# Performance work log

Hardware: AMD Instinct MI355X
Metric: run time of the kernel (lower is better)

## Reference

```python
import jax, jax.numpy as jnp
import numpy as np

N = 200000          # number of nodes (objects)
H = 64              # hidden_size
ARITIES = [1, 2, 3] # arity per relation
NTUP = [250000, 250000, 250000]  # ground atoms per relation


def setup_inputs() -> dict:
    key = jax.random.key(0)
    ks = jax.random.split(key, 32)
    inp = {"node_states": jax.random.normal(ks[0], (N, H), jnp.float32)}
    i = 1
    for r, (a, t) in enumerate(zip(ARITIES, NTUP)):
        inp[f"rel{r}_idx"] = jax.random.randint(ks[i], (t * a,), 0, N, dtype=jnp.int32).astype(jnp.int64); i += 1
        d = a * H
        s = (2.0 / d) ** 0.5
        inp[f"w1_r{r}"] = jax.random.normal(ks[i], (d, d), jnp.float32) * s; i += 1
        inp[f"b1_r{r}"] = jnp.zeros((d,), jnp.float32)
        inp[f"w2_r{r}"] = jax.random.normal(ks[i], (d, d), jnp.float32) * s; i += 1
        inp[f"b2_r{r}"] = jnp.zeros((d,), jnp.float32)
    su = (1.0 / (2 * H)) ** 0.5
    inp["wu1"] = jax.random.normal(ks[i], (2 * H, 2 * H), jnp.float32) * su; i += 1
    inp["bu1"] = jnp.zeros((2 * H,), jnp.float32)
    inp["wu2"] = jax.random.normal(ks[i], (2 * H, H), jnp.float32) * su
    inp["bu2"] = jnp.zeros((H,), jnp.float32)
    return inp


def reference(node_states, rel0_idx, rel1_idx, rel2_idx,
              w1_r0, b1_r0, w2_r0, b2_r0,
              w1_r1, b1_r1, w2_r1, b2_r1,
              w1_r2, b1_r2, w2_r2, b2_r2,
              wu1, bu1, wu2, bu2):
    sum_msg = jnp.zeros_like(node_states)
    rels = [(ARITIES[0], rel0_idx, w1_r0, b1_r0, w2_r0, b2_r0),
            (ARITIES[1], rel1_idx, w1_r1, b1_r1, w2_r1, b2_r1),
            (ARITIES[2], rel2_idx, w1_r2, b1_r2, w2_r2, b2_r2)]
    for a, idx, w1, b1, w2, b2 in rels:
        # gather node states for each ground atom: [T, a*H]
        x = node_states[idx].reshape(-1, a * H)
        h = jax.nn.relu(x @ w1 + b1)
        msg = (h @ w2 + b2).reshape(-1, H)  # [T*a, H]
        # scatter-add messages back to their nodes
        sum_msg = sum_msg.at[idx].add(msg)
    z = jnp.concatenate([sum_msg, node_states], axis=1)  # [N, 2H]
    return jax.nn.relu(z @ wu1 + bu1) @ wu2 + bu2
```

## Files before the change

kernel.cpp:

```cpp
#include <hip/hip_runtime.h>

#define H 64

typedef __attribute__((ext_vector_type(8))) __bf16 bf16x8;
typedef __attribute__((ext_vector_type(4))) float f32x4;
typedef unsigned short u16;
typedef unsigned int u32;

union F8 { bf16x8 b; u16 u[8]; uint4 q; };

__device__ __forceinline__ u16 f2bf(float f) {
    union { __bf16 h; u16 u; } v; v.h = (__bf16)f; return v.u;
}
__device__ __forceinline__ float bf2f(u16 x) {
    return __uint_as_float((u32)x << 16);
}
__device__ __forceinline__ unsigned swz(int col, int k, int K) {
    return ((unsigned)(col * K + k) * 2u) ^ (((unsigned)col & 7u) << 4);
}

struct Seg { const float* src; unsigned dstBytes; int K; int N; };
struct Segs { Seg s[8]; };

__global__ __launch_bounds__(256) void conv_weights(Segs segs, char* out) {
    Seg sg = segs.s[blockIdx.y];
    int total = sg.K * sg.N;
    char* dst = out + sg.dstBytes;
    for (int e = blockIdx.x * 256 + threadIdx.x; e < total; e += gridDim.x * 256) {
        int k = e / sg.N, n = e % sg.N;
        *(u16*)(dst + swz(n, k, sg.K)) = f2bf(sg.src[e]);
    }
}

__global__ __launch_bounds__(512) void scan_blocks(u32* __restrict__ data,
                                                   u32* __restrict__ sums, int n) {
    __shared__ u32 s[512];
    int tid = threadIdx.x, i = blockIdx.x * 512 + tid;
    u32 v = (i < n) ? data[i] : 0u;
    s[tid] = v; __syncthreads();
    for (int d = 1; d < 512; d <<= 1) {
        u32 t = (tid >= d) ? s[tid - d] : 0u; __syncthreads();
        s[tid] += t; __syncthreads();
    }
    if (i < n) data[i] = s[tid] - v;
    if (tid == 511) sums[blockIdx.x] = s[511];
}

__global__ __launch_bounds__(512) void scan_sums(u32* __restrict__ sums, int nb) {
    __shared__ u32 s[512];
    int tid = threadIdx.x;
    u32 v = (tid < nb) ? sums[tid] : 0u;
    s[tid] = v; __syncthreads();
    for (int d = 1; d < 512; d <<= 1) {
        u32 t = (tid >= d) ? s[tid - d] : 0u; __syncthreads();
        s[tid] += t; __syncthreads();
    }
    if (tid < nb) sums[tid] = s[tid] - v;
}

__global__ __launch_bounds__(512) void scan_add(u32* __restrict__ data,
                                                const u32* __restrict__ sums, int n) {
    int i = blockIdx.x * 512 + threadIdx.x;
    if (i < n) data[i] += sums[blockIdx.x];
}

struct OFix {
    const int* idx0; const int* idx1; const int* idx2;
    int m0, m1, m2;
    const u32* base; const u32* pre; u32* ord;
};

__global__ __launch_bounds__(256) void ord_fix(OFix a) {
    const int Mtot = a.m0 + a.m1 + a.m2;
    for (int e = blockIdx.x * 256 + threadIdx.x; e < Mtot; e += gridDim.x * 256) {
        int lm = e, node;
        if (lm < a.m0) node = a.idx0[lm];
        else { lm -= a.m0; if (lm < a.m1) node = a.idx1[lm]; else node = a.idx2[lm - a.m1]; }
        a.ord[a.base[node] + a.pre[e]] = (u32)e;
    }
}

template<int A>
__device__ __forceinline__ void msg_body(
    const float* __restrict__ ns, const int* __restrict__ idx,
    const u16* __restrict__ w1T, const float* __restrict__ b1,
    const u16* __restrict__ w2T, const float* __restrict__ b2,
    u16* __restrict__ msgR, int T, int bid, u16* Wl, u16* h1)
{
    constexpr int D   = A * 64;
    constexpr int KS  = D / 32;
    constexpr int NT  = D / 16;
    constexpr bool DUAL = (A == 1);
    constexpr int WH  = (A == 3) ? 3 : 1;
    constexpr int NTH = NT / WH;
    constexpr int COLH = D / WH;
    constexpr int NPF = (DUAL ? 2 * D * D : COLH * D) / 8 / 512;

    const int tid  = threadIdx.x;
    const int lane = tid & 63;
    const int w    = tid >> 6;
    const int g    = lane >> 4;
    const int lr   = lane & 15;

    const int tile = bid * 128;
    const int trow = tile + w * 16 + lr;
    const int tl   = trow < T ? trow : T - 1;

    auto stage = [&](const u16* gsrc) {
#pragma unroll
        for (int i = 0; i < NPF; ++i) {
            const u16* gp = gsrc + ((i * 512 + tid) << 3);
            u16* lp = Wl + ((i * 512 + (w << 6)) << 3);
            __builtin_amdgcn_global_load_lds(
                (const __attribute__((address_space(1))) void*)gp,
                (__attribute__((address_space(3))) void*)lp, 16, 0, 0);
        }
    };

    int nodes[A];
#pragma unroll
    for (int s = 0; s < A; ++s) nodes[s] = idx[(long)tl * A + s];

    bf16x8 a1[KS];
#pragma unroll
    for (int kk = 0; kk < KS; ++kk) {
        const float* p = ns + (long)nodes[kk >> 1] * H + ((kk & 1) * 32 + g * 8);
        float4 f0 = *(const float4*)p;
        float4 f1 = *(const float4*)(p + 4);
        F8 t;
        t.u[0] = f2bf(f0.x); t.u[1] = f2bf(f0.y); t.u[2] = f2bf(f0.z); t.u[3] = f2bf(f0.w);
        t.u[4] = f2bf(f1.x); t.u[5] = f2bf(f1.y); t.u[6] = f2bf(f1.z); t.u[7] = f2bf(f1.w);
        a1[kk] = t.b;
    }

    float bias1[NT], bias2[NT];
#pragma unroll
    for (int j = 0; j < NT; ++j) bias1[j] = b1[j * 16 + lr];
#pragma unroll
    for (int j = 0; j < NT; ++j) bias2[j] = b2[j * 16 + lr];

#pragma unroll
    for (int hh = 0; hh < WH; ++hh) {
        stage(DUAL ? w1T : (w1T + (size_t)hh * COLH * D));
        asm volatile("s_waitcnt vmcnt(0)" ::: "memory");
        __syncthreads();

#pragma unroll
        for (int j = 0; j < NTH; ++j) {
            const int jg = hh * NTH + j;
            f32x4 acc = {0.f, 0.f, 0.f, 0.f};
#pragma unroll
            for (int kk = 0; kk < KS; ++kk) {
                F8 bf; bf.q = *(const uint4*)((const char*)Wl + swz(j * 16 + lr, kk * 32 + g * 8, D));
                acc = __builtin_amdgcn_mfma_f32_16x16x32_bf16(a1[kk], bf.b, acc, 0, 0, 0);
            }
#pragma unroll
            for (int r = 0; r < 4; ++r) {
                float vv = acc[r] + bias1[jg];
                vv = vv > 0.f ? vv : 0.f;
                int row = w * 16 + g * 4 + r;
                *(u16*)((char*)h1 + swz(row, jg * 16 + lr, D)) = f2bf(vv);
            }
        }
        if constexpr (!DUAL) __syncthreads();
    }

    bf16x8 a2[KS];
#pragma unroll
    for (int kk = 0; kk < KS; ++kk) {
        int row = w * 16 + lr;
        F8 t; t.q = *(const uint4*)((const char*)h1 + swz(row, kk * 32 + g * 8, D));
        a2[kk] = t.b;
    }

#pragma unroll
    for (int hh = 0; hh < WH; ++hh) {
        if constexpr (!DUAL) {
            stage(w2T + (size_t)hh * COLH * D);
            asm volatile("s_waitcnt vmcnt(0)" ::: "memory");
            __syncthreads();
        }
        const char* W2base = DUAL ? (const char*)(Wl + D * D) : (const char*)Wl;

#pragma unroll
        for (int j = 0; j < NTH; ++j) {
            const int jg = hh * NTH + j;
            f32x4 acc = {0.f, 0.f, 0.f, 0.f};
#pragma unroll
            for (int kk = 0; kk < KS; ++kk) {
                F8 bf; bf.q = *(const uint4*)(W2base + swz(j * 16 + lr, kk * 32 + g * 8, D));
                acc = __builtin_amdgcn_mfma_f32_16x16x32_bf16(a2[kk], bf.b, acc, 0, 0, 0);
            }
            const int gc   = jg * 16 + lr;
            const int slot = gc >> 6;
            const int cs   = gc & 63;
#pragma unroll
            for (int r = 0; r < 4; ++r) {
                int la   = w * 16 + g * 4 + r;
                int mrow = la * A + slot;
                unsigned byte = (((unsigned)(mrow * 64 + cs)) * 2u) ^ (((unsigned)mrow & 7u) << 4);
                *(u16*)((char*)h1 + byte) = f2bf(acc[r] + bias2[jg]);
            }
        }
        if constexpr (!DUAL) { if (hh + 1 < WH) __syncthreads(); }
    }

    const int  mbase = (tile + w * 16) * A;
    const bool full  = (tile + 128 <= T);
#pragma unroll
    for (int i = 0; i < 16 * A; i += 4) {
        int ml   = i + (lane >> 4);
        int mrow = w * 16 * A + ml;
        bool ok  = full || ((tile + w * 16 + ml / A) < T);
        if (ok) {
            unsigned byte = (((unsigned)(mrow * 64 + (lane & 15) * 4)) * 2u) ^ (((unsigned)mrow & 7u) << 4);
            uint2 v = *(const uint2*)((const char*)h1 + byte);
            *(uint2*)(msgR + (size_t)(mbase + ml) * 64 + (lane & 15) * 4) = v;
        }
    }
}

struct MegaA {
    const float* ns;
    const int* idx0; const int* idx1; const int* idx2;
    int m0, m1, m2, t0, t1, t2;
    u32* cnt; u32* pre;
    const u16 *w10, *w20, *w11, *w21, *w12, *w22;
    const float *b10, *b20, *b11, *b21, *b12, *b22;
    u16* msgu;
    int nrank, nb2, nb1, nb0, striped;
};

__global__ __launch_bounds__(512, 4) void mega_kernel(MegaA a) {
    __shared__ __align__(16) u16 sm[36864];
    const int bx = blockIdx.x;
    int kind, id;
    if (a.striped) {
        const int strip = 4 * a.nrank;
        if (bx < strip) {
            if ((bx & 3) == 3) { kind = 1; id = bx >> 2; }
            else               { kind = 0; id = bx - (bx >> 2); }
        } else { kind = 0; id = bx - a.nrank; }
    } else {
        if (bx < a.nrank) { kind = 1; id = bx; }
        else              { kind = 0; id = bx - a.nrank; }
    }

    if (kind == 1) {
        const int Mtot = a.m0 + a.m1 + a.m2;
        for (int e = id * 512 + (int)threadIdx.x; e < Mtot; e += a.nrank * 512) {
            int lm = e, node;
            if (lm < a.m0) node = a.idx0[lm];
            else { lm -= a.m0; if (lm < a.m1) node = a.idx1[lm]; else node = a.idx2[lm - a.m1]; }
            a.pre[e] = atomicAdd(a.cnt + node, 1u);
        }
        return;
    }

    const int nmsg = a.nb2 + a.nb1 + a.nb0;
    if (id >= nmsg) return;
    if (id < a.nb2)
        msg_body<3>(a.ns, a.idx2, a.w12, a.b12, a.w22, a.b22,
                    a.msgu + (size_t)(a.m0 + a.m1) * 64, a.t2, id, sm, sm + 12288);
    else if (id < a.nb2 + a.nb1)
        msg_body<2>(a.ns, a.idx1, a.w11, a.b11, a.w21, a.b21,
                    a.msgu + (size_t)a.m0 * 64, a.t1, id - a.nb2, sm, sm + 16384);
    else
        msg_body<1>(a.ns, a.idx0, a.w10, a.b10, a.w20, a.b20,
                    a.msgu, a.t0, id - a.nb2 - a.nb1, sm, sm + 8192);
}

template<int A>
__global__ __launch_bounds__(512) void rel_kernel(
    const float* __restrict__ ns, const int* __restrict__ idx,
    const u16* __restrict__ w1T, const float* __restrict__ b1,
    const u16* __restrict__ w2T, const float* __restrict__ b2,
    float* __restrict__ dout, int T)
{
    constexpr int D  = A * 64;
    constexpr int KS = D / 32;
    constexpr int NT = D / 16;
    constexpr bool DUAL = (A == 1);
    __shared__ __align__(16) u16 Wl[(DUAL ? 2 : 1) * D * D];
    __shared__ __align__(16) u16 h1[128 * D];

    const int tid  = threadIdx.x;
    const int lane = tid & 63;
    const int w    = tid >> 6;
    const int g    = lane >> 4;
    const int lr   = lane & 15;

    const int tile = blockIdx.x * 128;
    const int trow = tile + w * 16 + lr;
    const int tl   = trow < T ? trow : T - 1;

    {
        constexpr int NV = (DUAL ? 2 : 1) * D * D / 8;
        const uint4* s4 = (const uint4*)w1T;
        uint4* d4 = (uint4*)Wl;
#pragma unroll
        for (int i = 0; i < NV / 512; ++i) d4[i * 512 + tid] = s4[i * 512 + tid];
    }

    int nodes[A];
#pragma unroll
    for (int s = 0; s < A; ++s) nodes[s] = idx[(long)tl * A + s];

    bf16x8 a1[KS];
#pragma unroll
    for (int kk = 0; kk < KS; ++kk) {
        const float* p = ns + (long)nodes[kk >> 1] * H + ((kk & 1) * 32 + g * 8);
        float4 f0 = *(const float4*)p;
        float4 f1 = *(const float4*)(p + 4);
        F8 t;
        t.u[0] = f2bf(f0.x); t.u[1] = f2bf(f0.y); t.u[2] = f2bf(f0.z); t.u[3] = f2bf(f0.w);
        t.u[4] = f2bf(f1.x); t.u[5] = f2bf(f1.y); t.u[6] = f2bf(f1.z); t.u[7] = f2bf(f1.w);
        a1[kk] = t.b;
    }

    float bias1[NT];
#pragma unroll
    for (int j = 0; j < NT; ++j) bias1[j] = b1[j * 16 + lr];

    __syncthreads();

#pragma unroll
    for (int j = 0; j < NT; ++j) {
        f32x4 acc = {0.f, 0.f, 0.f, 0.f};
#pragma unroll
        for (int kk = 0; kk < KS; ++kk) {
            F8 bf; bf.q = *(const uint4*)((const char*)Wl + swz(j * 16 + lr, kk * 32 + g * 8, D));
            acc = __builtin_amdgcn_mfma_f32_16x16x32_bf16(a1[kk], bf.b, acc, 0, 0, 0);
        }
#pragma unroll
        for (int r = 0; r < 4; ++r) {
            float vv = acc[r] + bias1[j];
            vv = vv > 0.f ? vv : 0.f;
            int row = w * 16 + g * 4 + r;
            *(u16*)((char*)h1 + swz(row, j * 16 + lr, D)) = f2bf(vv);
        }
    }

    const char* W2base;
    if constexpr (!DUAL) {
        __syncthreads();
        const uint4* s4 = (const uint4*)w2T;
        uint4* d4 = (uint4*)Wl;
        constexpr int NV = D * D / 8;
#pragma unroll
        for (int i = 0; i < NV / 512; ++i) d4[i * 512 + tid] = s4[i * 512 + tid];
        W2base = (const char*)Wl;
    } else {
        W2base = (const char*)(Wl + D * D);
    }

    bf16x8 a2[KS];
#pragma unroll
    for (int kk = 0; kk < KS; ++kk) {
        int row = w * 16 + lr;
        F8 t; t.q = *(const uint4*)((const char*)h1 + swz(row, kk * 32 + g * 8, D));
        a2[kk] = t.b;
    }

    float bias2[NT];
#pragma unroll
    for (int j = 0; j < NT; ++j) bias2[j] = b2[j * 16 + lr];

    int  nodes2[A][4];
    bool pred[4];
#pragma unroll
    for (int r = 0; r < 4; ++r) {
        int t  = tile + w * 16 + g * 4 + r;
        int tc = t < T ? t : T - 1;
        pred[r] = t < T;
#pragma unroll
        for (int s = 0; s < A; ++s) nodes2[s][r] = idx[(long)tc * A + s];
    }
    if constexpr (!DUAL) __syncthreads();

#pragma unroll
    for (int j = 0; j < NT; ++j) {
        f32x4 acc = {0.f, 0.f, 0.f, 0.f};
#pragma unroll
        for (int kk = 0; kk < KS; ++kk) {
            F8 bf; bf.q = *(const uint4*)(W2base + swz(j * 16 + lr, kk * 32 + g * 8, D));
            acc = __builtin_amdgcn_mfma_f32_16x16x32_bf16(a2[kk], bf.b, acc, 0, 0, 0);
        }
        const int slot = j >> 2;
        const int coff = (j & 3) * 16 + lr;
#pragma unroll
        for (int r = 0; r < 4; ++r) {
            if (pred[r])
                unsafeAtomicAdd(dout + (long)nodes2[slot][r] * H + coff, acc[r] + bias2[j]);
        }
    }
}

template<bool SEG>
__global__ __launch_bounds__(512) void update_kernel(
    const float* __restrict__ ns, const float* __restrict__ sum,
    const u32* __restrict__ ord, const u32* __restrict__ base,
    const u16* __restrict__ msg, int Mtot,
    const u16* __restrict__ wu1T, const float* __restrict__ bu1,
    const u16* __restrict__ wu2T, const float* __restrict__ bu2,
    float* __restrict__ out, int N)
{
    __shared__ __align__(16) u16 Wl[128 * 128 + 64 * 128];
    __shared__ __align__(16) u16 h[128 * 128];

    const int tid  = threadIdx.x;
    const int lane = tid & 63;
    const int w    = tid >> 6;
    const int g    = lane >> 4;
    const int lr   = lane & 15;

    {
        const uint4* s4 = (const uint4*)wu1T;
        uint4* d4 = (uint4*)Wl;
#pragma unroll
        for (int i = 0; i < 6; ++i) d4[i * 512 + tid] = s4[i * 512 + tid];
    }

    const int tile = blockIdx.x * 128;
    const int trow = tile + w * 16 + lr;
    const int tl   = trow < N ? trow : N - 1;

    bf16x8 a1[4];
    if constexpr (SEG) {
        const u32 s = base[tl];
        const u32 e = (tl + 1 < N) ? base[tl + 1] : (u32)Mtot;
        float s0[8], s1[8];
#pragma unroll
        for (int j = 0; j < 8; ++j) { s0[j] = 0.f; s1[j] = 0.f; }
        for (u32 p = s; p < e; ++p) {
            const u16* row = msg + (size_t)ord[p] * 64;
            F8 v0, v1;
            v0.q = *(const uint4*)(row + g * 8);
            v1.q = *(const uint4*)(row + 32 + g * 8);
#pragma unroll
            for (int j = 0; j < 8; ++j) { s0[j] += bf2f(v0.u[j]); s1[j] += bf2f(v1.u[j]); }
        }
        F8 t0, t1;
#pragma unroll
        for (int j = 0; j < 8; ++j) { t0.u[j] = f2bf(s0[j]); t1.u[j] = f2bf(s1[j]); }
        a1[0] = t0.b; a1[1] = t1.b;
    } else {
#pragma unroll
        for (int kk = 0; kk < 2; ++kk) {
            int k = kk * 32 + g * 8;
            const float* p = sum + (long)tl * H + k;
            float4 f0 = *(const float4*)p;
            float4 f1 = *(const float4*)(p + 4);
            F8 t;
            t.u[0] = f2bf(f0.x); t.u[1] = f2bf(f0.y); t.u[2] = f2bf(f0.z); t.u[3] = f2bf(f0.w);
            t.u[4] = f2bf(f1.x); t.u[5] = f2bf(f1.y); t.u[6] = f2bf(f1.z); t.u[7] = f2bf(f1.w);
            a1[kk] = t.b;
        }
    }
#pragma unroll
    for (int kk = 2; kk < 4; ++kk) {
        int k = (kk - 2) * 32 + g * 8;
        const float* p = ns + (long)tl * H + k;
        float4 f0 = *(const float4*)p;
        float4 f1 = *(const float4*)(p + 4);
        F8 t;
        t.u[0] = f2bf(f0.x); t.u[1] = f2bf(f0.y); t.u[2] = f2bf(f0.z); t.u[3] = f2bf(f0.w);
        t.u[4] = f2bf(f1.x); t.u[5] = f2bf(f1.y); t.u[6] = f2bf(f1.z); t.u[7] = f2bf(f1.w);
        a1[kk] = t.b;
    }

    float bias1[8], bias2[4];
#pragma unroll
    for (int j = 0; j < 8; ++j) bias1[j] = bu1[j * 16 + lr];
#pragma unroll
    for (int j = 0; j < 4; ++j) bias2[j] = bu2[j * 16 + lr];

    __syncthreads();

#pragma unroll
    for (int j = 0; j < 8; ++j) {
        f32x4 acc = {0.f, 0.f, 0.f, 0.f};
#pragma unroll
        for (int kk = 0; kk < 4; ++kk) {
            F8 bf; bf.q = *(const uint4*)((const char*)Wl + swz(j * 16 + lr, kk * 32 + g * 8, 128));
            acc = __builtin_amdgcn_mfma_f32_16x16x32_bf16(a1[kk], bf.b, acc, 0, 0, 0);
        }
#pragma unroll
        for (int r = 0; r < 4; ++r) {
            float vv = acc[r] + bias1[j];
            vv = vv > 0.f ? vv : 0.f;
            int row = w * 16 + g * 4 + r;
            *(u16*)((char*)h + swz(row, j * 16 + lr, 128)) = f2bf(vv);
        }
    }

    bf16x8 a2[4];
#pragma unroll
    for (int kk = 0; kk < 4; ++kk) {
        int row = w * 16 + lr;
        F8 t; t.q = *(const uint4*)((const char*)h + swz(row, kk * 32 + g * 8, 128));
        a2[kk] = t.b;
    }

    const char* W2base = (const char*)(Wl + 128 * 128);
#pragma unroll
    for (int j = 0; j < 4; ++j) {
        f32x4 acc = {0.f, 0.f, 0.f, 0.f};
#pragma unroll
        for (int kk = 0; kk < 4; ++kk) {
            F8 bf; bf.q = *(const uint4*)(W2base + swz(j * 16 + lr, kk * 32 + g * 8, 128));
            acc = __builtin_amdgcn_mfma_f32_16x16x32_bf16(a2[kk], bf.b, acc, 0, 0, 0);
        }
#pragma unroll
        for (int r = 0; r < 4; ++r) {
            int t = tile + w * 16 + g * 4 + r;
            if (t < N) out[(long)t * H + j * 16 + lr] = acc[r] + bias2[j];
        }
    }
}

extern "C" void kernel_launch(void* const* d_in, const int* in_sizes, int n_in,
                              void* d_out, int out_size, void* d_ws, size_t ws_size,
                              hipStream_t stream) {
    const float* ns = (const float*)d_in[0];
    const int* idxs[3] = { (const int*)d_in[1], (const int*)d_in[6], (const int*)d_in[11] };
    const float* b1s[3] = { (const float*)d_in[3], (const float*)d_in[8], (const float*)d_in[13] };
    const float* b2s[3] = { (const float*)d_in[5], (const float*)d_in[10], (const float*)d_in[15] };
    const float* bu1 = (const float*)d_in[17];
    const float* bu2 = (const float*)d_in[19];

    const int N = in_sizes[0] / H;
    const int Ts[3] = { in_sizes[1], in_sizes[6] / 2, in_sizes[11] / 3 };
    const int Ms[3] = { Ts[0] * 1, Ts[1] * 2, Ts[2] * 3 };
    const long Mtot = (long)Ms[0] + Ms[1] + Ms[2];

    char* wsb = (char*)d_ws;
    auto AL = [](size_t x) { return (x + 255) & ~(size_t)255; };

    const unsigned O_W1R0 = 0;
    const unsigned O_W2R0 = O_W1R0 + 64 * 64 * 2;
    const unsigned O_W1R1 = O_W2R0 + 64 * 64 * 2;
    const unsigned O_W2R1 = O_W1R1 + 128 * 128 * 2;
    const unsigned O_W1R2 = O_W2R1 + 128 * 128 * 2;
    const unsigned O_W2R2 = O_W1R2 + 192 * 192 * 2;
    const unsigned O_WU1  = O_W2R2 + 192 * 192 * 2;
    const unsigned O_WU2  = O_WU1 + 128 * 128 * 2;
    const size_t  wEnd    = O_WU2 + 128 * 64 * 2;
    const unsigned wOff1[3] = { O_W1R0, O_W1R1, O_W1R2 };
    const unsigned wOff2[3] = { O_W2R0, O_W2R1, O_W2R2 };

    const int nb = (N + 511) / 512;

    const size_t O_CNT = AL(wEnd);
    const size_t O_SUM = AL(O_CNT + (size_t)N * 4);
    const size_t O_PRE = AL(O_SUM + (size_t)nb * 4);
    const size_t O_ORD = AL(O_PRE + (size_t)Mtot * 4);
    const size_t O_MSG = AL(O_ORD + (size_t)Mtot * 4);
    const size_t need  = O_MSG + (size_t)Mtot * 128;

    const bool sorted = (nb <= 512) && (ws_size >= need);

    Segs segs;
    segs.s[0] = {(const float*)d_in[2],  O_W1R0, 64, 64};
    segs.s[1] = {(const float*)d_in[4],  O_W2R0, 64, 64};
    segs.s[2] = {(const float*)d_in[7],  O_W1R1, 128, 128};
    segs.s[3] = {(const float*)d_in[9],  O_W2R1, 128, 128};
    segs.s[4] = {(const float*)d_in[12], O_W1R2, 192, 192};
    segs.s[5] = {(const float*)d_in[14], O_W2R2, 192, 192};
    segs.s[6] = {(const float*)d_in[16], O_WU1, 128, 128};
    segs.s[7] = {(const float*)d_in[18], O_WU2, 128, 64};

    float* dout = (float*)d_out;
    const u16* W1[3] = { (const u16*)(wsb + wOff1[0]), (const u16*)(wsb + wOff1[1]), (const u16*)(wsb + wOff1[2]) };
    const u16* W2[3] = { (const u16*)(wsb + wOff2[0]), (const u16*)(wsb + wOff2[1]), (const u16*)(wsb + wOff2[2]) };

    auto gT = [](int T) { return (T + 127) / 128; };

    if (sorted) {
        u32* cnt = (u32*)(wsb + O_CNT);
        u32* sums = (u32*)(wsb + O_SUM);
        u32* pre = (u32*)(wsb + O_PRE);
        u32* ord = (u32*)(wsb + O_ORD);
        u16* msgu = (u16*)(wsb + O_MSG);

        hipMemsetAsync(cnt, 0, (size_t)N * 4, stream);
        conv_weights<<<dim3(36, 8), 256, 0, stream>>>(segs, wsb);

        const int nb0 = gT(Ts[0]), nb1 = gT(Ts[1]), nb2 = gT(Ts[2]);
        const int nmsg = nb0 + nb1 + nb2;
        int NR = nmsg / 3; if (NR > 1024) NR = 1024; if (NR < 1) NR = 1;
        const int striped = (nmsg >= 3 * NR) ? 1 : 0;
        const int NTOT = NR + nmsg;

        MegaA ma;
        ma.ns = ns;
        ma.idx0 = idxs[0]; ma.idx1 = idxs[1]; ma.idx2 = idxs[2];
        ma.m0 = Ms[0]; ma.m1 = Ms[1]; ma.m2 = Ms[2];
        ma.t0 = Ts[0]; ma.t1 = Ts[1]; ma.t2 = Ts[2];
        ma.cnt = cnt; ma.pre = pre;
        ma.w10 = W1[0]; ma.w20 = W2[0];
        ma.w11 = W1[1]; ma.w21 = W2[1];
        ma.w12 = W1[2]; ma.w22 = W2[2];
        ma.b10 = b1s[0]; ma.b20 = b2s[0];
        ma.b11 = b1s[1]; ma.b21 = b2s[1];
        ma.b12 = b1s[2]; ma.b22 = b2s[2];
        ma.msgu = msgu;
        ma.nrank = NR; ma.nb2 = nb2; ma.nb1 = nb1; ma.nb0 = nb0; ma.striped = striped;
        mega_kernel<<<NTOT, 512, 0, stream>>>(ma);

        scan_blocks<<<nb, 512, 0, stream>>>(cnt, sums, N);
        scan_sums<<<1, 512, 0, stream>>>(sums, nb);
        scan_add<<<nb, 512, 0, stream>>>(cnt, sums, N);

        OFix fx;
        fx.idx0 = idxs[0]; fx.idx1 = idxs[1]; fx.idx2 = idxs[2];
        fx.m0 = Ms[0]; fx.m1 = Ms[1]; fx.m2 = Ms[2];
        fx.base = cnt; fx.pre = pre; fx.ord = ord;
        ord_fix<<<2048, 256, 0, stream>>>(fx);

        update_kernel<true><<<(N + 127) / 128, 512, 0, stream>>>(
            ns, nullptr, ord, cnt, msgu, (int)Mtot,
            (const u16*)(wsb + O_WU1), bu1, (const u16*)(wsb + O_WU2), bu2, dout, N);
    } else {
        conv_weights<<<dim3(36, 8), 256, 0, stream>>>(segs, wsb);
        hipMemsetAsync(dout, 0, (size_t)N * H * sizeof(float), stream);
        for (int r = 0; r < 3; ++r) {
            const int T = Ts[r], nbl = gT(T);
            if (r == 0) rel_kernel<1><<<nbl, 512, 0, stream>>>(ns, idxs[0], W1[0], b1s[0], W2[0], b2s[0], dout, T);
            if (r == 1) rel_kernel<2><<<nbl, 512, 0, stream>>>(ns, idxs[1], W1[1], b1s[1], W2[1], b2s[1], dout, T);
            if (r == 2) rel_kernel<3><<<nbl, 512, 0, stream>>>(ns, idxs[2], W1[2], b1s[2], W2[2], b2s[2], dout, T);
        }
        update_kernel<false><<<(N + 127) / 128, 512, 0, stream>>>(
            ns, dout, nullptr, nullptr, nullptr, 0,
            (const u16*)(wsb + O_WU1), bu1, (const u16*)(wsb + O_WU2), bu2, dout, N);
    }
}
```

Measured before the change: 300.0 us.

## Pre-convert node states to bf16 and split waves into row/column groups

Adds a conv_nodes pass that converts node_states to bf16 once into the workspace, so the message and update kernels gather half as many bytes per row and skip per-gather conversion. For arity 2 and 3, each wave now computes two 16-row tiles over half the output column tiles, reusing each LDS weight fragment for two MFMAs. A block-wide cooperative store writes messages back to global memory. This adds an extra full pass over node states and more registers per wave, which may reduce occupancy.

```diff
diff --git a/kernel.cpp b/kernel.cpp
--- a/kernel.cpp
+++ b/kernel.cpp
@@ -29,6 +29,16 @@
     for (int e = blockIdx.x * 256 + threadIdx.x; e < total; e += gridDim.x * 256) {
         int k = e / sg.N, n = e % sg.N;
         *(u16*)(dst + swz(n, k, sg.K)) = f2bf(sg.src[e]);
+    }
+}
+
+__global__ __launch_bounds__(256) void conv_nodes(const float4* __restrict__ src,
+                                                  ushort4* __restrict__ dst, int n4) {
+    for (int i = blockIdx.x * 256 + threadIdx.x; i < n4; i += gridDim.x * 256) {
+        float4 f = src[i];
+        ushort4 o;
+        o.x = f2bf(f.x); o.y = f2bf(f.y); o.z = f2bf(f.z); o.w = f2bf(f.w);
+        dst[i] = o;
     }
 }
 
@@ -82,29 +92,33 @@
 
 template<int A>
 __device__ __forceinline__ void msg_body(
-    const float* __restrict__ ns, const int* __restrict__ idx,
+    const u16* __restrict__ nsb, const int* __restrict__ idx,
     const u16* __restrict__ w1T, const float* __restrict__ b1,
     const u16* __restrict__ w2T, const float* __restrict__ b2,
     u16* __restrict__ msgR, int T, int bid, u16* Wl, u16* h1)
 {
-    constexpr int D   = A * 64;
-    constexpr int KS  = D / 32;
-    constexpr int NT  = D / 16;
+    constexpr int D    = A * 64;
+    constexpr int KS   = D / 32;
+    constexpr int NT   = D / 16;
     constexpr bool DUAL = (A == 1);
-    constexpr int WH  = (A == 3) ? 3 : 1;
-    constexpr int NTH = NT / WH;
+    constexpr bool CS   = (A > 1);
+    constexpr int RF   = CS ? 2 : 1;
+    constexpr int WH   = (A == 3) ? 3 : 1;
+    constexpr int NTH  = NT / WH;
+    constexpr int NTW  = CS ? NTH / 2 : NTH;
     constexpr int COLH = D / WH;
-    constexpr int NPF = (DUAL ? 2 * D * D : COLH * D) / 8 / 512;
+    constexpr int NPF  = (DUAL ? 2 * D * D : COLH * D) / 8 / 512;
+    constexpr int NB   = WH * NTW;
 
     const int tid  = threadIdx.x;
     const int lane = tid & 63;
     const int w    = tid >> 6;
     const int g    = lane >> 4;
     const int lr   = lane & 15;
+    const int rg   = CS ? (w >> 1) : w;
+    const int cg   = CS ? (w & 1) : 0;
 
     const int tile = bid * 128;
-    const int trow = tile + w * 16 + lr;
-    const int tl   = trow < T ? trow : T - 1;
 
     auto stage = [&](const u16* gsrc) {
 #pragma unroll
@@ -117,27 +131,29 @@
         }
     };
 
-    int nodes[A];
-#pragma unroll
-    for (int s = 0; s < A; ++s) nodes[s] = idx[(long)tl * A + s];
-
-    bf16x8 a1[KS];
-#pragma unroll
-    for (int kk = 0; kk < KS; ++kk) {
-        const float* p = ns + (long)nodes[kk >> 1] * H + ((kk & 1) * 32 + g * 8);
-        float4 f0 = *(const float4*)p;
-        float4 f1 = *(const float4*)(p + 4);
-        F8 t;
-        t.u[0] = f2bf(f0.x); t.u[1] = f2bf(f0.y); t.u[2] = f2bf(f0.z); t.u[3] = f2bf(f0.w);
-        t.u[4] = f2bf(f1.x); t.u[5] = f2bf(f1.y); t.u[6] = f2bf(f1.z); t.u[7] = f2bf(f1.w);
-        a1[kk] = t.b;
-    }
-
-    float bias1[NT], bias2[NT];
-#pragma unroll
-    for (int j = 0; j < NT; ++j) bias1[j] = b1[j * 16 + lr];
-#pragma unroll
-    for (int j = 0; j < NT; ++j) bias2[j] = b2[j * 16 + lr];
+    bf16x8 a1[RF][KS];
+#pragma unroll
+    for (int rf = 0; rf < RF; ++rf) {
+        const int trow = tile + rg * (16 * RF) + rf * 16 + lr;
+        const int tl   = trow < T ? trow : T - 1;
+        int nodes[A];
+#pragma unroll
+        for (int s = 0; s < A; ++s) nodes[s] = idx[(long)tl * A + s];
+#pragma unroll
+        for (int kk = 0; kk < KS; ++kk) {
+            const u16* p = nsb + (long)nodes[kk >> 1] * H + ((kk & 1) * 32 + g * 8);
+            F8 t; t.q = *(const uint4*)p;
+            a1[rf][kk] = t.b;
+        }
+    }
+
+    float bias1[NB], bias2[NB];
+#pragma unroll
+    for (int i = 0; i < NB; ++i) {
+        const int jg = (i / NTW) * NTH + cg * NTW + (i % NTW);
+        bias1[i] = b1[jg * 16 + lr];
+        bias2[i] = b2[jg * 16 + lr];
+    }
 
 #pragma unroll
     for (int hh = 0; hh < WH; ++hh) {
@@ -146,31 +162,41 @@
         __syncthreads();
 
 #pragma unroll
-        for (int j = 0; j < NTH; ++j) {
-            const int jg = hh * NTH + j;
-            f32x4 acc = {0.f, 0.f, 0.f, 0.f};
+        for (int jl = 0; jl < NTW; ++jl) {
+            const int jc = cg * NTW + jl;
+            const int jg = hh * NTH + jc;
+            f32x4 acc0 = {0.f, 0.f, 0.f, 0.f};
+            f32x4 acc1 = {0.f, 0.f, 0.f, 0.f};
 #pragma unroll
             for (int kk = 0; kk < KS; ++kk) {
-                F8 bf; bf.q = *(const uint4*)((const char*)Wl + swz(j * 16 + lr, kk * 32 + g * 8, D));
-                acc = __builtin_amdgcn_mfma_f32_16x16x32_bf16(a1[kk], bf.b, acc, 0, 0, 0);
+                F8 bf; bf.q = *(const uint4*)((const char*)Wl + swz(jc * 16 + lr, kk * 32 + g * 8, D));
+                acc0 = __builtin_amdgcn_mfma_f32_16x16x32_bf16(a1[0][kk], bf.b, acc0, 0, 0, 0);
+                if constexpr (CS)
+                    acc1 = __builtin_amdgcn_mfma_f32_16x16x32_bf16(a1[1][kk], bf.b, acc1, 0, 0, 0);
             }
 #pragma unroll
             for (int r = 0; r < 4; ++r) {
-                float vv = acc[r] + bias1[jg];
-                vv = vv > 0.f ? vv : 0.f;
-                int row = w * 16 + g * 4 + r;
-                *(u16*)((char*)h1 + swz(row, jg * 16 + lr, D)) = f2bf(vv);
+                const int row0 = rg * (16 * RF) + g * 4 + r;
+                float v0 = acc0[r] + bias1[hh * NTW + jl]; v0 = v0 > 0.f ? v0 : 0.f;
+                *(u16*)((char*)h1 + swz(row0, jg * 16 + lr, D)) = f2bf(v0);
+                if constexpr (CS) {
+                    float v1 = acc1[r] + bias1[hh * NTW + jl]; v1 = v1 > 0.f ? v1 : 0.f;
+                    *(u16*)((char*)h1 + swz(row0 + 16, jg * 16 + lr, D)) = f2bf(v1);
+                }
             }
         }
         if constexpr (!DUAL) __syncthreads();
     }
 
-    bf16x8 a2[KS];
-#pragma unroll
-    for (int kk = 0; kk < KS; ++kk) {
-        int row = w * 16 + lr;
-        F8 t; t.q = *(const uint4*)((const char*)h1 + swz(row, kk * 32 + g * 8, D));
-        a2[kk] = t.b;
+    bf16x8 a2[RF][KS];
+#pragma unroll
+    for (int rf = 0; rf < RF; ++rf) {
+        const int row = rg * (16 * RF) + rf * 16 + lr;
+#pragma unroll
+        for (int kk = 0; kk < KS; ++kk) {
+            F8 t; t.q = *(const uint4*)((const char*)h1 + swz(row, kk * 32 + g * 8, D));
+            a2[rf][kk] = t.b;
+        }
     }
 
 #pragma unroll
@@ -183,45 +209,71 @@
         const char* W2base = DUAL ? (const char*)(Wl + D * D) : (const char*)Wl;
 
 #pragma unroll
-        for (int j = 0; j < NTH; ++j) {
-            const int jg = hh * NTH + j;
-            f32x4 acc = {0.f, 0.f, 0.f, 0.f};
+        for (int jl = 0; jl < NTW; ++jl) {
+            const int jc = cg * NTW + jl;
+            const int jg = hh * NTH + jc;
+            f32x4 acc0 = {0.f, 0.f, 0.f, 0.f};
+            f32x4 acc1 = {0.f, 0.f, 0.f, 0.f};
 #pragma unroll
             for (int kk = 0; kk < KS; ++kk) {
-                F8 bf; bf.q = *(const uint4*)(W2base + swz(j * 16 + lr, kk * 32 + g * 8, D));
-                acc = __builtin_amdgcn_mfma_f32_16x16x32_bf16(a2[kk], bf.b, acc, 0, 0, 0);
+                F8 bf; bf.q = *(const uint4*)(W2base + swz(jc * 16 + lr, kk * 32 + g * 8, D));
+                acc0 = __builtin_amdgcn_mfma_f32_16x16x32_bf16(a2[0][kk], bf.b, acc0, 0, 0, 0);
+                if constexpr (CS)
+                    acc1 = __builtin_amdgcn_mfma_f32_16x16x32_bf16(a2[1][kk], bf.b, acc1, 0, 0, 0);
             }
             const int gc   = jg * 16 + lr;
             const int slot = gc >> 6;
-            const int cs   = gc & 63;
+            const int cs_  = gc & 63;
 #pragma unroll
             for (int r = 0; r < 4; ++r) {
-                int la   = w * 16 + g * 4 + r;
-                int mrow = la * A + slot;
-                unsigned byte = (((unsigned)(mrow * 64 + cs)) * 2u) ^ (((unsigned)mrow & 7u) << 4);
-                *(u16*)((char*)h1 + byte) = f2bf(acc[r] + bias2[jg]);
+                const int a0 = rg * (16 * RF) + g * 4 + r;
+                const int m0 = a0 * A + slot;
+                unsigned b0 = (((unsigned)(m0 * 64 + cs_)) * 2u) ^ (((unsigned)m0 & 7u) << 4);
+                *(u16*)((char*)h1 + b0) = f2bf(acc0[r] + bias2[hh * NTW + jl]);
+                if constexpr (CS) {
+                    const int m1 = (a0 + 16) * A + slot;
+                    unsigned b1x = (((unsigned)(m1 * 64 + cs_)) * 2u) ^ (((unsigned)m1 & 7u) << 4);
+                    *(u16*)((char*)h1 + b1x) = f2bf(acc1[r] + bias2[hh * NTW + jl]);
+                }
             }
         }
         if constexpr (!DUAL) { if (hh + 1 < WH) __syncthreads(); }
     }
 
-    const int  mbase = (tile + w * 16) * A;
-    const bool full  = (tile + 128 <= T);
-#pragma unroll
-    for (int i = 0; i < 16 * A; i += 4) {
-        int ml   = i + (lane >> 4);
-        int mrow = w * 16 * A + ml;
-        bool ok  = full || ((tile + w * 16 + ml / A) < T);
-        if (ok) {
-            unsigned byte = (((unsigned)(mrow * 64 + (lane & 15) * 4)) * 2u) ^ (((unsigned)mrow & 7u) << 4);
-            uint2 v = *(const uint2*)((const char*)h1 + byte);
-            *(uint2*)(msgR + (size_t)(mbase + ml) * 64 + (lane & 15) * 4) = v;
+    if constexpr (CS) {
+        __syncthreads();
+        const int mbase = tile * A;
+        constexpr int CH = 128 * A * 16;
+#pragma unroll
+        for (int i = 0; i < CH / 512; ++i) {
+            const int c    = i * 512 + tid;
+            const int row  = c >> 4;
+            const int atom = row / A;
+            if (tile + atom < T) {
+                unsigned byte = (((unsigned)(row * 64 + (c & 15) * 4)) * 2u) ^ (((unsigned)row & 7u) << 4);
+                uint2 v = *(const uint2*)((const char*)h1 + byte);
+                *(uint2*)(msgR + (size_t)(mbase + row) * 64 + (c & 15) * 4) = v;
+            }
+        }
+    } else {
+        const int  mbase = (tile + w * 16) * A;
+        const bool full  = (tile + 128 <= T);
+#pragma unroll
+        for (int i = 0; i < 16 * A; i += 4) {
+            int ml   = i + (lane >> 4);
+            int mrow = w * 16 * A + ml;
+            bool ok  = full || ((tile + w * 16 + ml / A) < T);
+            if (ok) {
+                unsigned byte = (((unsigned)(mrow * 64 + (lane & 15) * 4)) * 2u) ^ (((unsigned)mrow & 7u) << 4);
+                uint2 v = *(const uint2*)((const char*)h1 + byte);
+                *(uint2*)(msgR + (size_t)((tile * A) + mrow) * 64 + (lane & 15) * 4) = v;
+            }
         }
     }
 }
 
 struct MegaA {
-    const float* ns;
+    const u16* nsb;
     const int* idx0; const int* idx1; const int* idx2;
     int m0, m1, m2, t0, t1, t2;
     u32* cnt; u32* pre;
@@ -260,13 +312,13 @@
     const int nmsg = a.nb2 + a.nb1 + a.nb0;
     if (id >= nmsg) return;
     if (id < a.nb2)
-        msg_body<3>(a.ns, a.idx2, a.w12, a.b12, a.w22, a.b22,
+        msg_body<3>(a.nsb, a.idx2, a.w12, a.b12, a.w22, a.b22,
                     a.msgu + (size_t)(a.m0 + a.m1) * 64, a.t2, id, sm, sm + 12288);
     else if (id < a.nb2 + a.nb1)
-        msg_body<2>(a.ns, a.idx1, a.w11, a.b11, a.w21, a.b21,
+        msg_body<2>(a.nsb, a.idx1, a.w11, a.b11, a.w21, a.b21,
                     a.msgu + (size_t)a.m0 * 64, a.t1, id - a.nb2, sm, sm + 16384);
     else
-        msg_body<1>(a.ns, a.idx0, a.w10, a.b10, a.w20, a.b20,
+        msg_body<1>(a.nsb, a.idx0, a.w10, a.b10, a.w20, a.b20,
                     a.msgu, a.t0, id - a.nb2 - a.nb1, sm, sm + 8192);
 }
 
@@ -396,9 +448,10 @@
     }
 }
 
-template<bool SEG>
+template<bool SEG, bool NSB>
 __global__ __launch_bounds__(512) void update_kernel(
-    const float* __restrict__ ns, const float* __restrict__ sum,
+    const float* __restrict__ ns, const u16* __restrict__ nsb,
+    const float* __restrict__ sum,
     const u32* __restrict__ ord, const u32* __restrict__ base,
     const u16* __restrict__ msg, int Mtot,
     const u16* __restrict__ wu1T, const float* __restrict__ bu1,
@@ -459,14 +512,20 @@
     }
 #pragma unroll
     for (int kk = 2; kk < 4; ++kk) {
-        int k = (kk - 2) * 32 + g * 8;
-        const float* p = ns + (long)tl * H + k;
-        float4 f0 = *(const float4*)p;
-        float4 f1 = *(const float4*)(p + 4);
-        F8 t;
-        t.u[0] = f2bf(f0.x); t.u[1] = f2bf(f0.y); t.u[2] = f2bf(f0.z); t.u[3] = f2bf(f0.w);
-        t.u[4] = f2bf(f1.x); t.u[5] = f2bf(f1.y); t.u[6] = f2bf(f1.z); t.u[7] = f2bf(f1.w);
-        a1[kk] = t.b;
+        if constexpr (NSB) {
+            const u16* prow = nsb + (long)tl * H;
+            F8 t; t.q = *(const uint4*)(prow + (kk - 2) * 32 + g * 8);
+            a1[kk] = t.b;
+        } else {
+            int k = (kk - 2) * 32 + g * 8;
+            const float* p = ns + (long)tl * H + k;
+            float4 f0 = *(const float4*)p;
+            float4 f1 = *(const float4*)(p + 4);
+            F8 t;
+            t.u[0] = f2bf(f0.x); t.u[1] = f2bf(f0.y); t.u[2] = f2bf(f0.z); t.u[3] = f2bf(f0.w);
+            t.u[4] = f2bf(f1.x); t.u[5] = f2bf(f1.y); t.u[6] = f2bf(f1.z); t.u[7] = f2bf(f1.w);
+            a1[kk] = t.b;
+        }
     }
 
     float bias1[8], bias2[4];
@@ -555,7 +614,9 @@
     const size_t O_SUM = AL(O_CNT + (size_t)N * 4);
     const size_t O_PRE = AL(O_SUM + (size_t)nb * 4);
     const size_t O_ORD = AL(O_PRE + (size_t)Mtot * 4);
-    const size_t O_MSG = AL(O_ORD + (size_t)Mtot * 4);
+    const size_t O_NSB = AL(O_ORD + (size_t)Mtot * 4);
+    const size_t nsLen = (size_t)N * H * 2;
+    const size_t O_MSG = AL(O_NSB + nsLen);
     const size_t need  = O_MSG + (size_t)Mtot * 128;
 
     const bool sorted = (nb <= 512) && (ws_size >= need);
@@ -581,10 +642,12 @@
         u32* sums = (u32*)(wsb + O_SUM);
         u32* pre = (u32*)(wsb + O_PRE);
         u32* ord = (u32*)(wsb + O_ORD);
+        u16* nsbp = (u16*)(wsb + O_NSB);
         u16* msgu = (u16*)(wsb + O_MSG);
 
         hipMemsetAsync(cnt, 0, (size_t)N * 4, stream);
         conv_weights<<<dim3(36, 8), 256, 0, stream>>>(segs, wsb);
+        conv_nodes<<<1024, 256, 0, stream>>>((const float4*)ns, (ushort4*)nsbp, N * H / 4);
 
         const int nb0 = gT(Ts[0]), nb1 = gT(Ts[1]), nb2 = gT(Ts[2]);
         const int nmsg = nb0 + nb1 + nb2;
@@ -593,7 +656,7 @@
         const int NTOT = NR + nmsg;
 
         MegaA ma;
-        ma.ns = ns;
+        ma.nsb = nsbp;
         ma.idx0 = idxs[0]; ma.idx1 = idxs[1]; ma.idx2 = idxs[2];
         ma.m0 = Ms[0]; ma.m1 = Ms[1]; ma.m2 = Ms[2];
         ma.t0 = Ts[0]; ma.t1 = Ts[1]; ma.t2 = Ts[2];
@@ -618,8 +681,8 @@
         fx.base = cnt; fx.pre = pre; fx.ord = ord;
         ord_fix<<<2048, 256, 0, stream>>>(fx);
 
-        update_kernel<true><<<(N + 127) / 128, 512, 0, stream>>>(
-            ns, nullptr, ord, cnt, msgu, (int)Mtot,
+        update_kernel<true, true><<<(N + 127) / 128, 512, 0, stream>>>(
+            ns, nsbp, nullptr, ord, cnt, msgu, (int)Mtot,
             (const u16*)(wsb + O_WU1), bu1, (const u16*)(wsb + O_WU2), bu2, dout, N);
     } else {
         conv_weights<<<dim3(36, 8), 256, 0, stream>>>(segs, wsb);
@@ -630,8 +693,8 @@
             if (r == 1) rel_kernel<2><<<nbl, 512, 0, stream>>>(ns, idxs[1], W1[1], b1s[1], W2[1], b2s[1], dout, T);
             if (r == 2) rel_kernel<3><<<nbl, 512, 0, stream>>>(ns, idxs[2], W1[2], b1s[2], W2[2], b2s[2], dout, T);
         }
-        update_kernel<false><<<(N + 127) / 128, 512, 0, stream>>>(
-            ns, dout, nullptr, nullptr, nullptr, 0,
+        update_kernel<false, false><<<(N + 127) / 128, 512, 0, stream>>>(
+            ns, nullptr, dout, nullptr, nullptr, nullptr, 0,
             (const u16*)(wsb + O_WU1), bu1, (const u16*)(wsb + O_WU2), bu2, dout, N);
     }
 }
```

New measurement: 271.3 us. 9.6% less time.
